# Optimization experiments

Measured on AMD Instinct MI355X. Metric: run time of the kernel, lower is better.

## Reference

```python
import jax, jax.numpy as jnp
import numpy as np

B, T, D_MODEL = 2, 2048, 2048
N, H, R = 1024, 16, 512
DH = 128          # mem_head_dim (even, fully rotated: rope_dim == DH)
MLAT = 128        # mem_latent_dim
TOPK = 64
EPS = 1e-6
ROPE_BASE = 10000.0


def _rms_norm(x, w):
    var = jnp.mean(jnp.square(x), axis=-1, keepdims=True)
    return x * jax.lax.rsqrt(var + EPS) * w


def _rotate_half(x):
    x1, x2 = jnp.split(x, 2, axis=-1)
    return jnp.concatenate([-x2, x1], axis=-1)


def _apply_rope(x, positions):
    # x: [B, H, L, DH], positions: [L] -> cos/sin [1, 1, L, DH]
    inv_freq = 1.0 / (ROPE_BASE ** (jnp.arange(0, DH, 2, dtype=jnp.float32) / DH))
    freqs = positions.astype(jnp.float32)[:, None] * inv_freq  # [L, DH/2]
    emb = jnp.concatenate([freqs, freqs], axis=-1)             # [L, DH]
    cos = jnp.cos(emb)[None, None].astype(x.dtype)
    sin = jnp.sin(emb)[None, None].astype(x.dtype)
    return x * cos + _rotate_half(x) * sin


def setup_inputs() -> dict:
    key = jax.random.key(0)
    ks = jax.random.split(key, 16)
    s = 0.02
    return {
        "x": jax.random.normal(ks[0], (B, T, D_MODEL), jnp.float32),
        "snapshots": jax.random.normal(ks[1], (B, N, H, R), jnp.float32),
        "snap_positions": jnp.sort(jax.random.randint(ks[2], (N,), 0, T)),
        "token_offset": 0,
        "Wq_down": jax.random.normal(ks[3], (D_MODEL, MLAT), jnp.float32) * s,
        "Wq_up": jax.random.normal(ks[4], (MLAT, H * DH), jnp.float32) * s,
        "Wg_down": jax.random.normal(ks[5], (D_MODEL, MLAT), jnp.float32) * s,
        "Wg_up": jax.random.normal(ks[6], (MLAT, H * DH), jnp.float32) * s,
        "Wo_down": jax.random.normal(ks[7], (H * DH, MLAT), jnp.float32) * s,
        "Wo_up": jax.random.normal(ks[8], (MLAT, D_MODEL), jnp.float32) * s,
        "Wk_up": jax.random.normal(ks[9], (R, DH), jnp.float32) * s,
        "Wv_up": jax.random.normal(ks[10], (R, DH), jnp.float32) * s,
        "q_norm_w": jnp.ones((DH,), jnp.float32),
        "k_norm_w": jnp.ones((DH,), jnp.float32),
        "sink_logit": jnp.zeros((H,), jnp.float32),
    }


def reference(x, snapshots, snap_positions, token_offset,
              Wq_down, Wq_up, Wg_down, Wg_up, Wo_down, Wo_up,
              Wk_up, Wv_up, q_norm_w, k_norm_w, sink_logit):
    b, t, d = x.shape
    _, n, h, r = snapshots.shape
    dh = DH

    # Q path: down/up projection, per-head RMSNorm -> [B, H, T, DH]
    q = ((x @ Wq_down) @ Wq_up).reshape(b, t, h, dh)
    q = _rms_norm(q, q_norm_w).transpose(0, 2, 1, 3)

    # K/V from snapshot latents: [B, N, H, DH] -> [B, H, N, DH]
    k = _rms_norm(snapshots @ Wk_up, k_norm_w).transpose(0, 2, 1, 3)
    v = (snapshots @ Wv_up).transpose(0, 2, 1, 3)

    # dual RoPE: Q by absolute token position, K by snapshot end position
    t_abs = token_offset + jnp.arange(t)
    q = _apply_rope(q, t_abs)
    k = _apply_rope(k, snap_positions)

    scores = jnp.einsum('bhtd,bhnd->bhtn', q, k) / jnp.sqrt(jnp.asarray(dh, q.dtype))

    # causal mask: snapshot strictly before token
    valid = (snap_positions[None, :] < t_abs[:, None])[None, None]  # [1,1,T,N]
    neg_inf = jnp.asarray(-jnp.inf, scores.dtype)
    scores = jnp.where(valid, scores, neg_inf)

    # causal top-k: keep entries >= k-th largest per (b,h,t)
    k_sel = min(TOPK, n)
    if k_sel < n:
        top_vals, _ = jax.lax.top_k(scores, k_sel)
        kth = top_vals[..., -1:]
        scores = jnp.where(scores >= kth, scores, neg_inf)

    # attention sink: extra learned logit per head
    sink = jnp.broadcast_to(sink_logit.astype(jnp.float32)[None, :, None, None], (b, h, t, 1))
    aug = jnp.concatenate([scores.astype(jnp.float32), sink], axis=-1)
    weights = jax.nn.softmax(aug, axis=-1)[..., :n].astype(v.dtype)

    out = jnp.einsum('bhtn,bhnd->bhtd', weights, v)
    out = out.transpose(0, 2, 1, 3).reshape(b, t, h * dh)

    gate = jax.nn.sigmoid((x @ Wg_down) @ Wg_up)
    out = out * gate
    out = (out @ Wo_down) @ Wo_up
    return out
```

## Files before the change

kernel.cpp:

```cpp
#include <hip/hip_runtime.h>

typedef unsigned short u16;
typedef unsigned int u32;
typedef __attribute__((ext_vector_type(8))) short bf16x8;
typedef __attribute__((ext_vector_type(8))) _Float16 f16x8;
typedef __attribute__((ext_vector_type(4))) float f32x4;

__device__ __forceinline__ float b2f(u16 u) {
  union { u32 i; float f; } v; v.i = ((u32)u) << 16; return v.f;
}
__device__ __forceinline__ u16 f2b(float f) {
  u32 u = __builtin_bit_cast(u32, f);
  u32 r = u + 0x7FFFu + ((u >> 16) & 1u);
  return (u16)(r >> 16);
}
__device__ __forceinline__ u16 f2h(float f) {
  return __builtin_bit_cast(u16, (_Float16)f);
}
__device__ __forceinline__ float h2f(u16 u) {
  return (float)__builtin_bit_cast(_Float16, u);
}
__device__ __forceinline__ float wsum(float v) {
  #pragma unroll
  for (int o = 32; o; o >>= 1) v += __shfl_xor(v, o);
  return v;
}
__device__ __forceinline__ float wmax(float v) {
  #pragma unroll
  for (int o = 32; o; o >>= 1) v = fmaxf(v, __shfl_xor(v, o));
  return v;
}

__global__ void k_detect(const u32* x, int* flag) {
  int lane = threadIdx.x;
  u32 w = x[lane * 131 + 7];
  float v = b2f((u16)(w & 0xFFFF));
  float a = fabsf(v);
  bool sane = (a > 1e-3f) && (a < 100.0f);
  unsigned long long m = __ballot(sane);
  if (lane == 0) flag[0] = (__popcll(m) >= 32) ? 0 : 1;
}

struct WtArgs {
  const void* s[8];
  const void* vq; const void* vk; const void* vs;
};
__global__ __launch_bounds__(256)
void k_wtrans_all(WtArgs a, u16* wb, const int* flag) {
  __shared__ u16 Ts[64][66];
  int id = blockIdx.x, t = threadIdx.x, dt = flag[0];
  if (id == 416) {
    u16* dq = wb + 1703936; u16* dk = wb + 1704064; u16* ds = wb + 1704192;
    if (t < 128) dq[t] = dt ? f2b(((const float*)a.vq)[t]) : ((const u16*)a.vq)[t];
    else if (t < 256) dk[t-128] = dt ? f2b(((const float*)a.vk)[t-128]) : ((const u16*)a.vk)[t-128];
    if (t < 16) ds[t] = dt ? f2b(((const float*)a.vs)[t]) : ((const u16*)a.vs)[t];
    return;
  }
  const int cum[9] = {0,64,128,144,160,224,288,352,416};
  const int gsh[8] = {1,1,1,1,5,5,1,5};
  const int Ks[8]  = {2048,2048,512,512,128,128,2048,128};
  const int Ns[8]  = {128,128,128,128,2048,2048,128,2048};
  const unsigned dsts[8] = {0,262144,524288,589824,655360,917504,1179648,1441792};
  int seg = 0;
  #pragma unroll
  for (int i = 0; i < 7; ++i) seg += (id >= cum[i+1]);
  int rel = id - cum[seg];
  int bx = rel & ((1 << gsh[seg]) - 1), by = rel >> gsh[seg];
  int K = Ks[seg], N = Ns[seg];
  const void* src = a.s[seg];
  u16* dst = wb + dsts[seg];
  int col0 = bx * 64, k0 = by * 64;
  int lr = t >> 4, lc = (t & 15) * 4;
  if (dt) {
    #pragma unroll
    for (int p = 0; p < 4; ++p) {
      int kr = lr + p * 16;
      float4 v = *(const float4*)((const float*)src + (size_t)(k0 + kr) * N + col0 + lc);
      Ts[kr][lc+0] = f2b(v.x); Ts[kr][lc+1] = f2b(v.y);
      Ts[kr][lc+2] = f2b(v.z); Ts[kr][lc+3] = f2b(v.w);
    }
  } else {
    #pragma unroll
    for (int p = 0; p < 4; ++p) {
      int kr = lr + p * 16;
      uint2 v = *(const uint2*)((const u16*)src + (size_t)(k0 + kr) * N + col0 + lc);
      *(uint2*)&Ts[kr][lc] = v;
    }
  }
  __syncthreads();
  int col = t >> 2, ks = (t & 3) * 16;
  u16 tmp[16];
  #pragma unroll
  for (int i = 0; i < 16; ++i) tmp[i] = Ts[ks + i][col];
  u16* dp = dst + (size_t)(col0 + col) * K + k0 + ks;
  *(uint4*)dp = *(uint4*)&tmp[0];
  *(uint4*)(dp + 8) = *(uint4*)&tmp[8];
}

template<int JW>
__device__ __forceinline__ void skinny_body(const void* A, const u16* BT, u16* C0, u16* C1,
    int K, bool a32, int m0, int tid, u16 (*As)[40]) {
  int wave = tid >> 6, lane = tid & 63, quad = lane >> 4, l16 = lane & 15;
  f32x4 acc[JW];
  #pragma unroll
  for (int j = 0; j < JW; ++j) acc[j] = (f32x4){0.f,0.f,0.f,0.f};
  int row32 = tid >> 4, kp32 = (tid & 15) * 2;
  int row16 = tid >> 2, kp16 = (tid & 3) * 8;
  float2 pf32 = {};
  uint4 pf16 = {};
  if (a32) pf32 = *(const float2*)((const float*)A + (size_t)(m0+row32)*K + kp32);
  else if (tid < 64) pf16 = *(const uint4*)((const u16*)A + (size_t)(m0+row16)*K + kp16);
  uint4 bf[JW];
  #pragma unroll
  for (int j = 0; j < JW; ++j) {
    int col = wave*(JW*16) + j*16 + l16;
    bf[j] = *(const uint4*)(BT + (size_t)col*K + quad*8);
  }
  for (int k0 = 0; k0 < K; k0 += 32) {
    if (a32) { As[row32][kp32] = f2b(pf32.x); As[row32][kp32+1] = f2b(pf32.y); }
    else if (tid < 64) *(uint4*)&As[row16][kp16] = pf16;
    __syncthreads();
    int k1 = k0 + 32;
    uint4 bn[JW];
    if (k1 < K) {
      if (a32) pf32 = *(const float2*)((const float*)A + (size_t)(m0+row32)*K + k1 + kp32);
      else if (tid < 64) pf16 = *(const uint4*)((const u16*)A + (size_t)(m0+row16)*K + k1 + kp16);
      #pragma unroll
      for (int j = 0; j < JW; ++j) {
        int col = wave*(JW*16) + j*16 + l16;
        bn[j] = *(const uint4*)(BT + (size_t)col*K + k1 + quad*8);
      }
    }
    bf16x8 af = *(const bf16x8*)&As[l16][quad*8];
    #pragma unroll
    for (int j = 0; j < JW; ++j)
      acc[j] = __builtin_amdgcn_mfma_f32_16x16x32_bf16(af, __builtin_bit_cast(bf16x8, bf[j]), acc[j], 0, 0, 0);
    __syncthreads();
    #pragma unroll
    for (int j = 0; j < JW; ++j) bf[j] = bn[j];
  }
  #pragma unroll
  for (int j = 0; j < JW; ++j) {
    int col = wave*(JW*16) + j*16 + l16;
    u16* Cp = (col < 128) ? C0 : C1;
    int cc = col & 127;
    #pragma unroll
    for (int r = 0; r < 4; ++r)
      Cp[(size_t)(m0 + quad*4 + r)*128 + cc] = f2b(acc[j][r]);
  }
}

__device__ __forceinline__ void gemm_up_body(const u16* A, const u16* BT, void* C, int ldc,
    bool o32, int m0, int n0, int tid, u16 (*As)[40]) {
  int wave = tid >> 6, lane = tid & 63, quad = lane >> 4, l16 = lane & 15;
  f32x4 acc[4] = {};
  int row = tid >> 2, kp = (tid & 3) * 8;
  uint4 pa = *(const uint4*)(A + (size_t)(m0+row)*128 + kp);
  uint4 bf[4];
  #pragma unroll
  for (int j = 0; j < 4; ++j)
    bf[j] = *(const uint4*)(BT + (size_t)(n0 + j*16 + l16)*128 + quad*8);
  #pragma unroll
  for (int k0 = 0; k0 < 128; k0 += 32) {
    *(uint4*)&As[row][kp] = pa;
    __syncthreads();
    uint4 bn[4];
    if (k0 < 96) {
      pa = *(const uint4*)(A + (size_t)(m0+row)*128 + k0 + 32 + kp);
      #pragma unroll
      for (int j = 0; j < 4; ++j)
        bn[j] = *(const uint4*)(BT + (size_t)(n0 + j*16 + l16)*128 + k0 + 32 + quad*8);
    }
    bf16x8 af = *(const bf16x8*)&As[wave*16 + l16][quad*8];
    #pragma unroll
    for (int j = 0; j < 4; ++j)
      acc[j] = __builtin_amdgcn_mfma_f32_16x16x32_bf16(af, __builtin_bit_cast(bf16x8, bf[j]), acc[j], 0, 0, 0);
    __syncthreads();
    #pragma unroll
    for (int j = 0; j < 4; ++j) bf[j] = bn[j];
  }
  #pragma unroll
  for (int j = 0; j < 4; ++j) {
    #pragma unroll
    for (int r = 0; r < 4; ++r) {
      size_t ci = (size_t)(m0 + wave*16 + quad*4 + r)*ldc + n0 + j*16 + l16;
      float v = acc[j][r];
      if (o32) ((float*)C)[ci] = v; else ((u16*)C)[ci] = f2b(v);
    }
  }
}

__device__ __forceinline__ void kpost_body(const u16* kraw, u16* kT, const u16* kw,
                                           const int* spos, int rel, int tid) {
  int wave = tid >> 6, lane = tid & 63;
  int rr = rel * 4 + wave;
  int n = (rr >> 4) & 1023, b = rr >> 14, h = rr & 15;
  size_t base = (size_t)rr * 128;
  float x0 = b2f(kraw[base + lane]);
  float x1 = b2f(kraw[base + lane + 64]);
  float ss = wsum(x0*x0 + x1*x1);
  float inv = rsqrtf(ss * (1.0f/128.0f) + 1e-6f);
  float y0 = x0 * inv * b2f(kw[lane]);
  float y1 = x1 * inv * b2f(kw[lane + 64]);
  float pos = (float)spos[n];
  float invf = __expf(-(float)lane * (9.210340371976184f / 64.0f));
  float sn, cs; sincosf(pos * invf, &sn, &cs);
  size_t ob = ((size_t)(b*16 + h) * 1024 + n) * 128;
  kT[ob + lane]      = f2b(y0*cs - y1*sn);
  kT[ob + lane + 64] = f2b(y1*cs + y0*sn);
}

__device__ __forceinline__ void vtrans_body(const u16* vraw, u16* vtt, int bid, int t,
                                            u16 (*Vs)[136]) {
  int ng = bid & 15, bh = bid >> 4;
  int b = bh >> 4, h = bh & 15;
  int n0 = ng * 64;
  int li = t >> 4, seg = (t & 15) * 8;
  #pragma unroll
  for (int p = 0; p < 4; ++p) {
    int i = li + p * 16;
    size_t row = (size_t)(b*1024 + n0 + i) * 16 + h;
    *(uint4*)&Vs[i][seg] = *(const uint4*)(vraw + row*128 + seg);
  }
  __syncthreads();
  int dh = t >> 1, nh = (t & 1) * 32;
  u16 outv[32];
  #pragma unroll
  for (int i = 0; i < 32; ++i) outv[i] = f2h(b2f(Vs[nh + i][dh]));
  u16* dst = vtt + ((size_t)bh * 128 + dh) * 1024 + n0 + nh;
  *(uint4*)(dst)      = *(uint4*)&outv[0];
  *(uint4*)(dst + 8)  = *(uint4*)&outv[8];
  *(uint4*)(dst + 16) = *(uint4*)&outv[16];
  *(uint4*)(dst + 24) = *(uint4*)&outv[24];
}

__global__ __launch_bounds__(256)
void k_down_all(const void* x, const void* snap, const u16* BdT, const u16* BkvT,
                u16* qlat, u16* glat, u16* kraw, u16* vraw, const int* flag) {
  __shared__ u16 As[16][40];
  int id = blockIdx.x;
  bool a32 = flag[0] != 0;
  if (id < 256) skinny_body<4>(x, BdT, qlat, glat, 2048, a32, id*16, threadIdx.x, As);
  else          skinny_body<4>(snap, BkvT, kraw, vraw, 512, a32, (id-256)*16, threadIdx.x, As);
}

__global__ __launch_bounds__(256)
void k_mid_all(const u16* qlat, const u16* glat, const u16* WquT, const u16* WguT,
               u16* qraw, u16* graw, const u16* kraw, u16* kT, const u16* vraw, u16* vtt,
               const u16* ckw, const int* spos, const int* flag) {
  __shared__ u16 smem[64*136];
  int id = blockIdx.x, tid = threadIdx.x;
  if (id < 4096) {
    u16 (*As)[40] = (u16 (*)[40])smem;
    int rel = id & 2047;
    const u16* A  = (id < 2048) ? qlat : glat;
    const u16* BT = (id < 2048) ? WquT : WguT;
    u16* C        = (id < 2048) ? qraw : graw;
    gemm_up_body(A, BT, C, 2048, false, (rel >> 5) * 64, (rel & 31) * 64, tid, As);
  } else if (id < 12288) {
    kpost_body(kraw, kT, ckw, spos, id - 4096, tid);
  } else {
    vtrans_body(vraw, vtt, id - 12288, tid, (u16 (*)[136])smem);
  }
}

__global__ __launch_bounds__(256)
void k_olat(const u16* Ao, const u16* WodT, u16* olat, const int* flag) {
  __shared__ u16 As[16][40];
  skinny_body<2>(Ao, WodT, olat, olat, 2048, false, blockIdx.x*16, threadIdx.x, As);
}

__global__ __launch_bounds__(256)
void k_gemm_up(const u16* A, const u16* BT, void* C, int ldc, const int* flag, int out_dyn) {
  __shared__ u16 As[64][40];
  gemm_up_body(A, BT, C, ldc, out_dyn && flag[0], blockIdx.y*64, blockIdx.x*64, threadIdx.x, As);
}

__global__ __launch_bounds__(256, 4)
void k_attn(const u16* qraw, const u16* kT, const u16* vtt, const u16* graw,
            const int* spos, const int* tok, const u16* sink, const u16* qw, u16* o) {
  __shared__ u16 sc[16*1024];
  __shared__ int pos_s[1024];
  __shared__ float rz_s[16];
  char* scB = (char*)sc;
  u16 (*Qs)[136] = (u16 (*)[136])sc;

  int tid = threadIdx.x;
  int wave = tid >> 6, lane = tid & 63, quad = lane >> 4, l16 = lane & 15;
  int bid0 = blockIdx.x;
  int bid = (bid0 & 7) * 512 + (bid0 >> 3);
  int tile = bid & 127, bh = bid >> 7;
  int h = bh & 15, b = bh >> 4;
  int t0 = tile * 16;
  int tok0 = tok[0];

  ((int4*)pos_s)[tid] = ((const int4*)spos)[tid];

  {
    float qw0 = b2f(qw[lane]), qw1 = b2f(qw[lane + 64]);
    float invf = __expf(-(float)lane * (9.210340371976184f / 64.0f));
    #pragma unroll 1
    for (int s = 0; s < 4; ++s) {
      int i = wave*4 + s;
      size_t base = ((size_t)(b*2048 + t0 + i))*2048 + h*128;
      float x0 = b2f(qraw[base + lane]);
      float x1 = b2f(qraw[base + lane + 64]);
      float ss = wsum(x0*x0 + x1*x1);
      float inv = rsqrtf(ss * (1.0f/128.0f) + 1e-6f);
      float y0 = x0 * inv * qw0;
      float y1 = x1 * inv * qw1;
      float pos = (float)(tok0 + t0 + i);
      float sn, cs; sincosf(pos * invf, &sn, &cs);
      Qs[i][lane]      = f2b(y0*cs - y1*sn);
      Qs[i][lane + 64] = f2b(y1*cs + y0*sn);
    }
  }
  __syncthreads();

  int nmax;
  {
    int lim = tok0 + t0 + 15;
    int lo = 0, hi = 1024;
    #pragma unroll 1
    while (lo < hi) { int mid = (lo + hi) >> 1; if (pos_s[mid] < lim) lo = mid + 1; else hi = mid; }
    nmax = lo;
  }
  int pmax = (nmax + 63) >> 6;
  int kkmax = (nmax + 31) >> 5;

  bf16x8 af[4];
  #pragma unroll
  for (int ks = 0; ks < 4; ++ks) af[ks] = *(const bf16x8*)&Qs[l16][ks*32 + quad*8];
  __syncthreads();

  const u16* kTb = kT + (size_t)bh * 131072;
  int nrow = wave*16 + l16;
  uint4 kf[4];
  if (pmax > 0) {
    const u16* kr = kTb + (size_t)nrow * 128 + quad*8;
    #pragma unroll
    for (int ks = 0; ks < 4; ++ks) kf[ks] = *(const uint4*)(kr + ks*32);
  }
  int lim0 = tok0 + t0;
  #pragma unroll 1
  for (int p = 0; p < pmax; ++p) {
    uint4 kn[4];
    if (p + 1 < pmax) {
      const u16* kr = kTb + (size_t)((p+1)*64 + nrow) * 128 + quad*8;
      #pragma unroll
      for (int ks = 0; ks < 4; ++ks) kn[ks] = *(const uint4*)(kr + ks*32);
    }
    f32x4 c = {};
    __builtin_amdgcn_s_setprio(1);
    #pragma unroll
    for (int ks = 0; ks < 4; ++ks)
      c = __builtin_amdgcn_mfma_f32_16x16x32_bf16(af[ks], __builtin_bit_cast(bf16x8, kf[ks]), c, 0, 0, 0);
    __builtin_amdgcn_s_setprio(0);
    int n = p*64 + nrow;
    int pn = pos_s[n];
    #pragma unroll
    for (int r = 0; r < 4; ++r) {
      int t = quad*4 + r;
      float s = c[r] * 0.08838834764831845f;
      if (pn >= lim0 + t) s = -INFINITY;
      *(u16*)(scB + ((t*2048 + n*2) ^ ((t&7)<<4))) = f2h(s);
    }
    #pragma unroll
    for (int ks = 0; ks < 4; ++ks) kf[ks] = kn[ks];
  }
  __syncthreads();

  float sinkv = b2f(sink[h]);

  int tl0 = wave*4;
  int c0 = lane*8;
  #pragma unroll 1
  for (int half = 0; half < 2; ++half) {
    float sv[2][16]; int key[2][16];
    #pragma unroll
    for (int s2 = 0; s2 < 2; ++s2) {
      int tl = tl0 + half*2 + s2;
      int sxor = (tl&7) << 4;
      const char* rowp = scB + tl*2048;
      uint4 r0 = *(const uint4*)(rowp + ((lane*16) ^ sxor));
      uint4 r1 = *(const uint4*)(rowp + (1024 + ((lane*16) ^ sxor)));
      #pragma unroll
      for (int j = 0; j < 8; ++j) {
        sv[s2][j]   = (c0 + j       < nmax) ? h2f(((const u16*)&r0)[j]) : -INFINITY;
        sv[s2][j+8] = (c0 + j + 512 < nmax) ? h2f(((const u16*)&r1)[j]) : -INFINITY;
      }
    }
    float mx[2];
    #pragma unroll
    for (int s2 = 0; s2 < 2; ++s2) {
      float m = -INFINITY;
      #pragma unroll
      for (int j = 0; j < 16; ++j) {
        float f = sv[s2][j];
        m = fmaxf(m, f);
        float fs = fminf(fmaxf(f * 256.0f + 2048.0f, 0.0f), 4095.0f);
        key[s2][j] = (int)fs;
      }
      mx[s2] = m;
    }
    #pragma unroll
    for (int os = 32; os; os >>= 1) {
      #pragma unroll
      for (int s2 = 0; s2 < 2; ++s2) mx[s2] = fmaxf(mx[s2], __shfl_xor(mx[s2], os));
    }
    int lo2[2] = {0, 0}, hi2[2] = {4096, 4096};
    #pragma unroll 1
    for (int it = 0; it < 12; ++it) {
      #pragma unroll
      for (int s2 = 0; s2 < 2; ++s2) {
        int mid = (lo2[s2] + hi2[s2]) >> 1;
        int c = 0;
        #pragma unroll
        for (int j = 0; j < 16; ++j) c += (int)__popcll(__ballot(key[s2][j] >= mid));
        if (c >= 64) lo2[s2] = mid; else hi2[s2] = mid;
      }
    }
    float m2[2], zp[2];
    u16 wq[2][16];
    #pragma unroll
    for (int s2 = 0; s2 < 2; ++s2) {
      m2[s2] = fmaxf(mx[s2], sinkv);
      float z = 0.f;
      #pragma unroll
      for (int j = 0; j < 16; ++j) {
        float e = (key[s2][j] >= lo2[s2] && sv[s2][j] > -1e37f) ? __expf(sv[s2][j] - m2[s2]) : 0.f;
        z += e;
        wq[s2][j] = f2h(e);
      }
      zp[s2] = z;
    }
    #pragma unroll
    for (int os = 32; os; os >>= 1) {
      #pragma unroll
      for (int s2 = 0; s2 < 2; ++s2) zp[s2] += __shfl_xor(zp[s2], os);
    }
    #pragma unroll
    for (int s2 = 0; s2 < 2; ++s2) {
      int tl = tl0 + half*2 + s2;
      float Z = zp[s2] + __expf(sinkv - m2[s2]);
      if (lane == 0) rz_s[tl] = 1.0f / Z;
      int sxor = (tl&7) << 4;
      char* rowp = scB + tl*2048;
      *(uint4*)(rowp + ((lane*16) ^ sxor))        = *(uint4*)&wq[s2][0];
      *(uint4*)(rowp + (1024 + ((lane*16) ^ sxor))) = *(uint4*)&wq[s2][8];
    }
  }
  __syncthreads();

  const u16* vbase = vtt + (size_t)bh * 131072;
  int dh0 = wave * 32;
  const u16* vr0 = vbase + (size_t)(dh0 + l16)*1024 + quad*8;
  const u16* vr1 = vbase + (size_t)(dh0 + 16 + l16)*1024 + quad*8;
  f32x4 acc0 = {}, acc1 = {};
  uint4 vf0 = *(const uint4*)vr0;
  uint4 vf1 = *(const uint4*)vr1;
  int axor = (l16&7) << 4;
  const char* arow = scB + l16*2048;
  #pragma unroll 1
  for (int kk = 0; kk < kkmax; ++kk) {
    uint4 vn0, vn1;
    if (kk + 1 < kkmax) {
      vn0 = *(const uint4*)(vr0 + (kk+1)*32);
      vn1 = *(const uint4*)(vr1 + (kk+1)*32);
    }
    f16x8 a = *(const f16x8*)(arow + ((kk*64 + quad*16) ^ axor));
    __builtin_amdgcn_s_setprio(1);
    acc0 = __builtin_amdgcn_mfma_f32_16x16x32_f16(a, __builtin_bit_cast(f16x8, vf0), acc0, 0, 0, 0);
    acc1 = __builtin_amdgcn_mfma_f32_16x16x32_f16(a, __builtin_bit_cast(f16x8, vf1), acc1, 0, 0, 0);
    __builtin_amdgcn_s_setprio(0);
    vf0 = vn0; vf1 = vn1;
  }

  #pragma unroll
  for (int r = 0; r < 4; ++r) {
    int t = quad*4 + r;
    float rz = rz_s[t];
    size_t oi = ((size_t)(b*2048 + t0 + t))*2048 + h*128 + dh0 + l16;
    float g0 = 1.0f / (1.0f + __expf(-b2f(graw[oi])));
    float g1 = 1.0f / (1.0f + __expf(-b2f(graw[oi + 16])));
    o[oi] = f2b(acc0[r] * rz * g0);
    o[oi + 16] = f2b(acc1[r] * rz * g1);
  }
}

extern "C" void kernel_launch(void* const* d_in, const int* in_sizes, int n_in,
                              void* d_out, int out_size, void* d_ws, size_t ws_size,
                              hipStream_t stream) {
  char* ws = (char*)d_ws;
  int* flag = (int*)(ws + 0);
  u16* wb = (u16*)(ws + 4096);

  u16* BdT  = wb + 0;
  u16* BkvT = wb + 524288;
  u16* WquT = wb + 655360;
  u16* WguT = wb + 917504;
  u16* WodT = wb + 1179648;
  u16* WouT = wb + 1441792;
  u16* cqw  = wb + 1703936;
  u16* ckw  = wb + 1704064;
  u16* csink= wb + 1704192;

  const size_t O_QLAT = 4198400;
  const size_t O_GLAT = 5246976;
  const size_t O_QRAW = 6295552;
  const size_t O_GRAW = 23072768;
  const size_t O_KRAW = 39849984;
  const size_t O_VRAW = 48238592;
  const size_t O_KT   = 56627200;
  const size_t O_VTT  = 65015808;

  const int* spos = (const int*)d_in[2];
  const int* tok  = (const int*)d_in[3];

  k_detect<<<1, 64, 0, stream>>>((const u32*)d_in[0], flag);

  WtArgs wa;
  wa.s[0] = d_in[4];  wa.s[1] = d_in[6];  wa.s[2] = d_in[10]; wa.s[3] = d_in[11];
  wa.s[4] = d_in[5];  wa.s[5] = d_in[7];  wa.s[6] = d_in[8];  wa.s[7] = d_in[9];
  wa.vq = d_in[12]; wa.vk = d_in[13]; wa.vs = d_in[14];
  k_wtrans_all<<<417, 256, 0, stream>>>(wa, wb, flag);

  k_down_all<<<2304, 256, 0, stream>>>(d_in[0], d_in[1], BdT, BkvT,
      (u16*)(ws + O_QLAT), (u16*)(ws + O_GLAT), (u16*)(ws + O_KRAW), (u16*)(ws + O_VRAW), flag);

  k_mid_all<<<12800, 256, 0, stream>>>((const u16*)(ws + O_QLAT), (const u16*)(ws + O_GLAT),
      WquT, WguT, (u16*)(ws + O_QRAW), (u16*)(ws + O_GRAW),
      (const u16*)(ws + O_KRAW), (u16*)(ws + O_KT), (const u16*)(ws + O_VRAW), (u16*)(ws + O_VTT),
      ckw, spos, flag);

  k_attn<<<4096, 256, 0, stream>>>((const u16*)(ws + O_QRAW), (const u16*)(ws + O_KT),
      (const u16*)(ws + O_VTT), (const u16*)(ws + O_GRAW), spos, tok, csink, cqw,
      (u16*)(ws + O_GRAW));

  k_olat<<<256, 256, 0, stream>>>((const u16*)(ws + O_GRAW), WodT, (u16*)(ws + O_QLAT), flag);
  k_gemm_up<<<dim3(32,64), 256, 0, stream>>>((const u16*)(ws + O_QLAT), WouT, d_out, 2048, flag, 1);
}
```

Measured before the change: 521.9 us.

## Cut attention LDS use, specialize softmax/top-k by key count, prefetch gate

Removes the shared-memory copy of snapshot positions and the rz scratch, reading positions from global memory and storing per-row normalizers in a global workspace buffer. The aim is to shrink LDS so five blocks per CU can be resident. The top-k/softmax phase is templated so rows with at most 512 valid keys process only half the columns, and the 12-step threshold search is skipped when there are no more than 64 valid keys. Gate values and normalizers are loaded before the PV loop to hide latency. The trade-off is extra global/L2 traffic for positions and normalizers, plus code duplication.

```diff
diff --git a/kernel.cpp b/kernel.cpp
--- a/kernel.cpp
+++ b/kernel.cpp
@@ -276,12 +276,100 @@
   gemm_up_body(A, BT, C, ldc, out_dyn && flag[0], blockIdx.y*64, blockIdx.x*64, threadIdx.x, As);
 }
 
-__global__ __launch_bounds__(256, 4)
+template<int NJ>
+__device__ __forceinline__ void attn_phase2(char* scB, float* rzb, int tl0, int lane,
+                                            int nmax, float sinkv, bool do_search) {
+  int c0 = lane * 8;
+  #pragma unroll 1
+  for (int half = 0; half < 2; ++half) {
+    float sv[2][NJ]; int key[2][NJ];
+    #pragma unroll
+    for (int s2 = 0; s2 < 2; ++s2) {
+      int tl = tl0 + half*2 + s2;
+      int sxor = (tl & 7) << 4;
+      const char* rowp = scB + tl*2048;
+      uint4 r0 = *(const uint4*)(rowp + ((lane*16) ^ sxor));
+      #pragma unroll
+      for (int j = 0; j < 8; ++j)
+        sv[s2][j] = (c0 + j < nmax) ? h2f(((const u16*)&r0)[j]) : -INFINITY;
+      if constexpr (NJ == 16) {
+        uint4 r1 = *(const uint4*)(rowp + (1024 + ((lane*16) ^ sxor)));
+        #pragma unroll
+        for (int j = 0; j < 8; ++j)
+          sv[s2][j+8] = (c0 + j + 512 < nmax) ? h2f(((const u16*)&r1)[j]) : -INFINITY;
+      }
+    }
+    float mx[2];
+    #pragma unroll
+    for (int s2 = 0; s2 < 2; ++s2) {
+      float m = -INFINITY;
+      #pragma unroll
+      for (int j = 0; j < NJ; ++j) {
+        float f = sv[s2][j];
+        m = fmaxf(m, f);
+        float fs = fminf(fmaxf(f * 256.0f + 2048.0f, 0.0f), 4095.0f);
+        key[s2][j] = (int)fs;
+      }
+      mx[s2] = m;
+    }
+    #pragma unroll
+    for (int os = 32; os; os >>= 1) {
+      mx[0] = fmaxf(mx[0], __shfl_xor(mx[0], os));
+      mx[1] = fmaxf(mx[1], __shfl_xor(mx[1], os));
+    }
+    int lo2[2] = {0, 0};
+    if (do_search) {
+      int hi2[2] = {4096, 4096};
+      #pragma unroll 1
+      for (int it = 0; it < 12; ++it) {
+        #pragma unroll
+        for (int s2 = 0; s2 < 2; ++s2) {
+          int mid = (lo2[s2] + hi2[s2]) >> 1;
+          int c = 0;
+          #pragma unroll
+          for (int j = 0; j < NJ; ++j) c += (int)__popcll(__ballot(key[s2][j] >= mid));
+          if (c >= 64) lo2[s2] = mid; else hi2[s2] = mid;
+        }
+      }
+    }
+    float m2[2], zp[2];
+    u16 wq[2][16];
+    #pragma unroll
+    for (int s2 = 0; s2 < 2; ++s2) {
+      m2[s2] = fmaxf(mx[s2], sinkv);
+      float z = 0.f;
+      #pragma unroll
+      for (int j = 0; j < NJ; ++j) {
+        float e = (key[s2][j] >= lo2[s2] && sv[s2][j] > -1e37f) ? __expf(sv[s2][j] - m2[s2]) : 0.f;
+        z += e;
+        wq[s2][j] = f2h(e);
+      }
+      zp[s2] = z;
+    }
+    #pragma unroll
+    for (int os = 32; os; os >>= 1) {
+      zp[0] += __shfl_xor(zp[0], os);
+      zp[1] += __shfl_xor(zp[1], os);
+    }
+    #pragma unroll
+    for (int s2 = 0; s2 < 2; ++s2) {
+      int tl = tl0 + half*2 + s2;
+      float Z = zp[s2] + __expf(sinkv - m2[s2]);
+      if (lane == 0) rzb[tl] = 1.0f / Z;
+      int sxor = (tl & 7) << 4;
+      char* rowp = scB + tl*2048;
+      *(uint4*)(rowp + ((lane*16) ^ sxor)) = *(uint4*)&wq[s2][0];
+      if constexpr (NJ == 16)
+        *(uint4*)(rowp + (1024 + ((lane*16) ^ sxor))) = *(uint4*)&wq[s2][8];
+    }
+  }
+}
+
+__global__ __launch_bounds__(256, 5)
 void k_attn(const u16* qraw, const u16* kT, const u16* vtt, const u16* graw,
-            const int* spos, const int* tok, const u16* sink, const u16* qw, u16* o) {
+            const int* spos, const int* tok, const u16* sink, const u16* qw,
+            float* rzg, u16* o) {
   __shared__ u16 sc[16*1024];
-  __shared__ int pos_s[1024];
-  __shared__ float rz_s[16];
   char* scB = (char*)sc;
   u16 (*Qs)[136] = (u16 (*)[136])sc;
 
@@ -293,8 +381,7 @@
   int h = bh & 15, b = bh >> 4;
   int t0 = tile * 16;
   int tok0 = tok[0];
-
-  ((int4*)pos_s)[tid] = ((const int4*)spos)[tid];
+  float* rzb = rzg + bid * 16;
 
   {
     float qw0 = b2f(qw[lane]), qw1 = b2f(qw[lane + 64]);
@@ -322,7 +409,7 @@
     int lim = tok0 + t0 + 15;
     int lo = 0, hi = 1024;
     #pragma unroll 1
-    while (lo < hi) { int mid = (lo + hi) >> 1; if (pos_s[mid] < lim) lo = mid + 1; else hi = mid; }
+    while (lo < hi) { int mid = (lo + hi) >> 1; if (spos[mid] < lim) lo = mid + 1; else hi = mid; }
     nmax = lo;
   }
   int pmax = (nmax + 63) >> 6;
@@ -336,19 +423,23 @@
   const u16* kTb = kT + (size_t)bh * 131072;
   int nrow = wave*16 + l16;
   uint4 kf[4];
+  int pn = 0;
   if (pmax > 0) {
     const u16* kr = kTb + (size_t)nrow * 128 + quad*8;
     #pragma unroll
     for (int ks = 0; ks < 4; ++ks) kf[ks] = *(const uint4*)(kr + ks*32);
+    pn = spos[nrow];
   }
   int lim0 = tok0 + t0;
   #pragma unroll 1
   for (int p = 0; p < pmax; ++p) {
     uint4 kn[4];
+    int pn_next = 0;
     if (p + 1 < pmax) {
       const u16* kr = kTb + (size_t)((p+1)*64 + nrow) * 128 + quad*8;
       #pragma unroll
       for (int ks = 0; ks < 4; ++ks) kn[ks] = *(const uint4*)(kr + ks*32);
+      pn_next = spos[(p+1)*64 + nrow];
     }
     f32x4 c = {};
     __builtin_amdgcn_s_setprio(1);
@@ -357,7 +448,6 @@
       c = __builtin_amdgcn_mfma_f32_16x16x32_bf16(af[ks], __builtin_bit_cast(bf16x8, kf[ks]), c, 0, 0, 0);
     __builtin_amdgcn_s_setprio(0);
     int n = p*64 + nrow;
-    int pn = pos_s[n];
     #pragma unroll
     for (int r = 0; r < 4; ++r) {
       int t = quad*4 + r;
@@ -367,93 +457,31 @@
     }
     #pragma unroll
     for (int ks = 0; ks < 4; ++ks) kf[ks] = kn[ks];
+    pn = pn_next;
   }
   __syncthreads();
 
   float sinkv = b2f(sink[h]);
 
   int tl0 = wave*4;
-  int c0 = lane*8;
-  #pragma unroll 1
-  for (int half = 0; half < 2; ++half) {
-    float sv[2][16]; int key[2][16];
-    #pragma unroll
-    for (int s2 = 0; s2 < 2; ++s2) {
-      int tl = tl0 + half*2 + s2;
-      int sxor = (tl&7) << 4;
-      const char* rowp = scB + tl*2048;
-      uint4 r0 = *(const uint4*)(rowp + ((lane*16) ^ sxor));
-      uint4 r1 = *(const uint4*)(rowp + (1024 + ((lane*16) ^ sxor)));
-      #pragma unroll
-      for (int j = 0; j < 8; ++j) {
-        sv[s2][j]   = (c0 + j       < nmax) ? h2f(((const u16*)&r0)[j]) : -INFINITY;
-        sv[s2][j+8] = (c0 + j + 512 < nmax) ? h2f(((const u16*)&r1)[j]) : -INFINITY;
-      }
-    }
-    float mx[2];
-    #pragma unroll
-    for (int s2 = 0; s2 < 2; ++s2) {
-      float m = -INFINITY;
-      #pragma unroll
-      for (int j = 0; j < 16; ++j) {
-        float f = sv[s2][j];
-        m = fmaxf(m, f);
-        float fs = fminf(fmaxf(f * 256.0f + 2048.0f, 0.0f), 4095.0f);
-        key[s2][j] = (int)fs;
-      }
-      mx[s2] = m;
-    }
-    #pragma unroll
-    for (int os = 32; os; os >>= 1) {
-      #pragma unroll
-      for (int s2 = 0; s2 < 2; ++s2) mx[s2] = fmaxf(mx[s2], __shfl_xor(mx[s2], os));
-    }
-    int lo2[2] = {0, 0}, hi2[2] = {4096, 4096};
-    #pragma unroll 1
-    for (int it = 0; it < 12; ++it) {
-      #pragma unroll
-      for (int s2 = 0; s2 < 2; ++s2) {
-        int mid = (lo2[s2] + hi2[s2]) >> 1;
-        int c = 0;
-        #pragma unroll
-        for (int j = 0; j < 16; ++j) c += (int)__popcll(__ballot(key[s2][j] >= mid));
-        if (c >= 64) lo2[s2] = mid; else hi2[s2] = mid;
-      }
-    }
-    float m2[2], zp[2];
-    u16 wq[2][16];
-    #pragma unroll
-    for (int s2 = 0; s2 < 2; ++s2) {
-      m2[s2] = fmaxf(mx[s2], sinkv);
-      float z = 0.f;
-      #pragma unroll
-      for (int j = 0; j < 16; ++j) {
-        float e = (key[s2][j] >= lo2[s2] && sv[s2][j] > -1e37f) ? __expf(sv[s2][j] - m2[s2]) : 0.f;
-        z += e;
-        wq[s2][j] = f2h(e);
-      }
-      zp[s2] = z;
-    }
-    #pragma unroll
-    for (int os = 32; os; os >>= 1) {
-      #pragma unroll
-      for (int s2 = 0; s2 < 2; ++s2) zp[s2] += __shfl_xor(zp[s2], os);
-    }
-    #pragma unroll
-    for (int s2 = 0; s2 < 2; ++s2) {
-      int tl = tl0 + half*2 + s2;
-      float Z = zp[s2] + __expf(sinkv - m2[s2]);
-      if (lane == 0) rz_s[tl] = 1.0f / Z;
-      int sxor = (tl&7) << 4;
-      char* rowp = scB + tl*2048;
-      *(uint4*)(rowp + ((lane*16) ^ sxor))        = *(uint4*)&wq[s2][0];
-      *(uint4*)(rowp + (1024 + ((lane*16) ^ sxor))) = *(uint4*)&wq[s2][8];
-    }
-  }
+  bool do_search = (nmax > 64);
+  if (nmax > 512) attn_phase2<16>(scB, rzb, tl0, lane, nmax, sinkv, do_search);
+  else            attn_phase2<8> (scB, rzb, tl0, lane, nmax, sinkv, do_search);
   __syncthreads();
 
+  int dh0 = wave * 32;
+  float rz4[4];
+  u16 g0r[4], g1r[4];
+  #pragma unroll
+  for (int r = 0; r < 4; ++r) {
+    int t = quad*4 + r;
+    rz4[r] = rzb[t];
+    size_t oi = ((size_t)(b*2048 + t0 + t))*2048 + h*128 + dh0 + l16;
+    g0r[r] = graw[oi];
+    g1r[r] = graw[oi + 16];
+  }
+
   const u16* vbase = vtt + (size_t)bh * 131072;
-  int dh0 = wave * 32;
   const u16* vr0 = vbase + (size_t)(dh0 + l16)*1024 + quad*8;
   const u16* vr1 = vbase + (size_t)(dh0 + 16 + l16)*1024 + quad*8;
   f32x4 acc0 = {}, acc1 = {};
@@ -479,12 +507,11 @@
   #pragma unroll
   for (int r = 0; r < 4; ++r) {
     int t = quad*4 + r;
-    float rz = rz_s[t];
     size_t oi = ((size_t)(b*2048 + t0 + t))*2048 + h*128 + dh0 + l16;
-    float g0 = 1.0f / (1.0f + __expf(-b2f(graw[oi])));
-    float g1 = 1.0f / (1.0f + __expf(-b2f(graw[oi + 16])));
-    o[oi] = f2b(acc0[r] * rz * g0);
-    o[oi + 16] = f2b(acc1[r] * rz * g1);
+    float g0 = 1.0f / (1.0f + __expf(-b2f(g0r[r])));
+    float g1 = 1.0f / (1.0f + __expf(-b2f(g1r[r])));
+    o[oi] = f2b(acc0[r] * rz4[r] * g0);
+    o[oi + 16] = f2b(acc1[r] * rz4[r] * g1);
   }
 }
 
@@ -535,7 +562,7 @@
 
   k_attn<<<4096, 256, 0, stream>>>((const u16*)(ws + O_QRAW), (const u16*)(ws + O_KT),
       (const u16*)(ws + O_VTT), (const u16*)(ws + O_GRAW), spos, tok, csink, cqw,
-      (u16*)(ws + O_GRAW));
+      (float*)(ws + O_GLAT), (u16*)(ws + O_GRAW));
 
   k_olat<<<256, 256, 0, stream>>>((const u16*)(ws + O_GRAW), WodT, (u16*)(ws + O_QLAT), flag);
   k_gemm_up<<<dim3(32,64), 256, 0, stream>>>((const u16*)(ws + O_QLAT), WouT, d_out, 2048, flag, 1);
```

After: 507.2 us. 2.8% less time.
